# Optimization experiments

Hardware: AMD Instinct MI355X
Metric: run time of the kernel (lower is better)

The kernel has to match this reference:

```python
import jax, jax.numpy as jnp
import numpy as np

VOCAB, EMBED, HIDDEN = 32000, 256, 512
B, S = 64, 64


def setup_inputs() -> dict:
    key = jax.random.key(0)
    ks = jax.random.split(key, 10)
    target_seq = jax.random.randint(ks[0], (B, S), 0, VOCAB)
    context = jax.random.normal(ks[1], (B, HIDDEN), dtype=jnp.float32)
    h = jax.random.normal(ks[2], (B, HIDDEN), dtype=jnp.float32)
    c = jax.random.normal(ks[3], (B, HIDDEN), dtype=jnp.float32)
    # parameters (torch default-ish init scale)
    emb_table = jax.random.normal(ks[4], (VOCAB, EMBED), dtype=jnp.float32)
    k_lstm = 1.0 / np.sqrt(HIDDEN)
    w_ih = jax.random.uniform(ks[5], (4 * HIDDEN, EMBED + HIDDEN), minval=-k_lstm, maxval=k_lstm, dtype=jnp.float32)
    w_hh = jax.random.uniform(ks[6], (4 * HIDDEN, HIDDEN), minval=-k_lstm, maxval=k_lstm, dtype=jnp.float32)
    b_ih = jax.random.uniform(ks[7], (4 * HIDDEN,), minval=-k_lstm, maxval=k_lstm, dtype=jnp.float32)
    b_hh = jnp.zeros((4 * HIDDEN,), dtype=jnp.float32)
    k_fc = 1.0 / np.sqrt(2 * HIDDEN)
    w_fc = jax.random.uniform(ks[8], (VOCAB, 2 * HIDDEN), minval=-k_fc, maxval=k_fc, dtype=jnp.float32)
    b_fc = jax.random.uniform(ks[9], (VOCAB,), minval=-k_fc, maxval=k_fc, dtype=jnp.float32)
    return dict(target_seq=target_seq, context=context, h=h, c=c,
                emb_table=emb_table, w_ih=w_ih, w_hh=w_hh, b_ih=b_ih, b_hh=b_hh,
                w_fc=w_fc, b_fc=b_fc)


def _decode(target_seq, context, h, c, emb_table, w_ih, w_hh, b_ih, b_hh, w_fc, b_fc):
    # teacher_forcing_ratio = 1.0 -> input at step t is target_seq[:, t]
    emb = emb_table[target_seq]                                    # [B,S,E]
    ctx_t = jnp.broadcast_to(context[:, None, :], (emb.shape[0], emb.shape[1], context.shape[1]))
    lstm_in = jnp.concatenate([emb, ctx_t], axis=-1)               # [B,S,E+H]
    # precompute input-to-hidden part of gates for all steps
    pre = jnp.einsum('bsf,gf->bsg', lstm_in, w_ih) + b_ih + b_hh   # [B,S,4H]
    H = h.shape[1]

    def step(carry, pre_t):
        h_t, c_t = carry
        gates = pre_t + h_t @ w_hh.T                               # [B,4H]
        i, f, g, o = jnp.split(gates, 4, axis=-1)
        i, f, o = jax.nn.sigmoid(i), jax.nn.sigmoid(f), jax.nn.sigmoid(o)
        g = jnp.tanh(g)
        c_n = f * c_t + i * g
        h_n = o * jnp.tanh(c_n)
        return (h_n, c_n), h_n

    _, hs = jax.lax.scan(step, (h, c), jnp.swapaxes(pre, 0, 1))    # hs: [S,B,H]
    hs = jnp.swapaxes(hs, 0, 1)                                    # [B,S,H]
    out_in = jnp.concatenate([hs, ctx_t], axis=-1)                 # [B,S,2H]
    logits = jnp.einsum('bsf,vf->bsv', out_in, w_fc) + b_fc        # [B,S,V]
    return logits


def reference(target_seq, context, h, c, emb_table, w_ih, w_hh, b_ih, b_hh, w_fc, b_fc):
    return _decode(target_seq, context, h, c, emb_table, w_ih, w_hh, b_ih, b_hh, w_fc, b_fc)
```

## Files before the change

### kernel.cpp

```cpp
#include <hip/hip_runtime.h>
#include <hip/hip_bf16.h>

#define VOCAB 32000
#define EMBED 256
#define HIDDEN 512
#define BB 64
#define SS 64
#define M_ROWS (BB * SS)
#define G4 (4 * HIDDEN)
#define NBLK 16
#define NTOT 256
#define NTILE_N (VOCAB / 256)
#define CHUNK 5
#define NCHUNK (NTILE_N / CHUNK)
#define NITEM (SS * NCHUNK)

typedef __attribute__((ext_vector_type(8))) short short8v;
typedef __attribute__((ext_vector_type(4))) float float4v;
typedef __attribute__((ext_vector_type(4))) unsigned int uint4v;

__device__ __forceinline__ ushort f2bf(float f) {
    union { float f; unsigned u; } v; v.f = f;
    unsigned r = (v.u + 0x7FFFu + ((v.u >> 16) & 1u)) >> 16;
    return (ushort)r;
}

__device__ __forceinline__ float fast_tanh(float x) {
    float xc = fminf(fmaxf(x, -15.f), 15.f);
    float e = __expf(2.f * xc);
    return (e - 1.f) / (e + 1.f);
}

__device__ __forceinline__ void glds16(const ushort* g, ushort* l) {
    __builtin_amdgcn_global_load_lds(
        (const __attribute__((address_space(1))) unsigned int*)(const void*)g,
        (__attribute__((address_space(3))) unsigned int*)(void*)l, 16, 0, 0);
}

__global__ void k_conv_strided(const float* __restrict__ in, ushort* __restrict__ out,
                               int lg2cols, int instride, int n8) {
    int i = blockIdx.x * blockDim.x + threadIdx.x;
    int stride = gridDim.x * blockDim.x;
    int colmask = (1 << lg2cols) - 1;
    for (; i < n8; i += stride) {
        int i8 = i << 3;
        int row = i8 >> lg2cols, col = i8 & colmask;
        const float* src = in + (size_t)row * instride + col;
        float4 v0 = *(const float4*)src;
        float4 v1 = *(const float4*)(src + 4);
        short8v o;
        o[0] = (short)f2bf(v0.x); o[1] = (short)f2bf(v0.y);
        o[2] = (short)f2bf(v0.z); o[3] = (short)f2bf(v0.w);
        o[4] = (short)f2bf(v1.x); o[5] = (short)f2bf(v1.y);
        o[6] = (short)f2bf(v1.z); o[7] = (short)f2bf(v1.w);
        *(short8v*)(out + i8) = o;
    }
}

__global__ void k_build_emb(const int* __restrict__ tseq, const float* __restrict__ emb,
                            ushort* __restrict__ embbf) {
    int rid = blockIdx.x * 8 + (threadIdx.x >> 5);
    int c0 = (threadIdx.x & 31) * 8;
    int tok = tseq[rid];
    const float* src = emb + (size_t)tok * EMBED + c0;
    float4 v0 = *(const float4*)src;
    float4 v1 = *(const float4*)(src + 4);
    short8v o;
    o[0] = (short)f2bf(v0.x); o[1] = (short)f2bf(v0.y);
    o[2] = (short)f2bf(v0.z); o[3] = (short)f2bf(v0.w);
    o[4] = (short)f2bf(v1.x); o[5] = (short)f2bf(v1.y);
    o[6] = (short)f2bf(v1.z); o[7] = (short)f2bf(v1.w);
    *(short8v*)(embbf + (size_t)rid * EMBED + c0) = o;
}

__global__ void k_prep_small(const float* __restrict__ b_ih, const float* __restrict__ b_hh,
                             float* __restrict__ bias_pre,
                             const float* __restrict__ h0, ushort* __restrict__ hbufA,
                             const float* __restrict__ ctx, ushort* __restrict__ ctx_bf,
                             unsigned* __restrict__ ctrl) {
    int i = blockIdx.x * blockDim.x + threadIdx.x;
    if (i < 1024) ctrl[i] = 0;
    if (i < G4) bias_pre[i] = b_ih[i] + b_hh[i];
    if (i < BB * HIDDEN) {
        hbufA[i] = f2bf(h0[i]);
        ctx_bf[i] = f2bf(ctx[i]);
    }
}

__global__ __launch_bounds__(256) void k_gemm_smallM(
    const ushort* __restrict__ Abf, const float* __restrict__ Wf, int wstride,
    const float* __restrict__ bias, float* __restrict__ Cout, int N) {
    int t = threadIdx.x;
    int wv = t >> 6, lane = t & 63, lr = lane & 15, kg = lane >> 4;
    int bcol = blockIdx.x * 128;

    float4v acc[4][2];
#pragma unroll
    for (int m = 0; m < 4; m++)
#pragma unroll
        for (int n = 0; n < 2; n++) acc[m][n] = (float4v){0.f, 0.f, 0.f, 0.f};

#pragma unroll 4
    for (int ks = 0; ks < 16; ks++) {
        short8v a[4];
#pragma unroll
        for (int m = 0; m < 4; m++)
            a[m] = *(const short8v*)(Abf + (size_t)(m * 16 + lr) * 512 + ks * 32 + kg * 8);
        short8v w[2];
#pragma unroll
        for (int n = 0; n < 2; n++) {
            const float* src = Wf + (size_t)(bcol + wv * 32 + n * 16 + lr) * wstride + ks * 32 + kg * 8;
            float4 v0 = *(const float4*)src;
            float4 v1 = *(const float4*)(src + 4);
            short8v w8;
            w8[0] = (short)f2bf(v0.x); w8[1] = (short)f2bf(v0.y);
            w8[2] = (short)f2bf(v0.z); w8[3] = (short)f2bf(v0.w);
            w8[4] = (short)f2bf(v1.x); w8[5] = (short)f2bf(v1.y);
            w8[6] = (short)f2bf(v1.z); w8[7] = (short)f2bf(v1.w);
            w[n] = w8;
        }
#pragma unroll
        for (int m = 0; m < 4; m++)
#pragma unroll
            for (int n = 0; n < 2; n++)
                acc[m][n] = __builtin_amdgcn_mfma_f32_16x16x32_bf16(a[m], w[n], acc[m][n], 0, 0, 0);
    }

#pragma unroll
    for (int n = 0; n < 2; n++) {
        int col = bcol + wv * 32 + n * 16 + lr;
        float bv = bias[col];
#pragma unroll
        for (int m = 0; m < 4; m++) {
            int row = m * 16 + kg * 4;
#pragma unroll
            for (int j = 0; j < 4; j++)
                Cout[(size_t)(row + j) * N + col] = acc[m][n][j] + bv;
        }
    }
}

__global__ __launch_bounds__(512) void k_gemm_bf16(
    const ushort* __restrict__ A, const ushort* __restrict__ W,
    const float* __restrict__ rowbias, float* __restrict__ C,
    int M, int N, int K) {
    __shared__ ushort As[256 * 32];
    __shared__ ushort Ws[256 * 32];
    int t = threadIdx.x;

    int gx = N >> 8, gy = M >> 8;
    int nwg = gx * gy;
    int q = nwg >> 3, r = nwg & 7;
    int xcd = blockIdx.x & 7, idx = blockIdx.x >> 3;
    int wg = (xcd < r) ? xcd * (q + 1) + idx : r * (q + 1) + (xcd - r) * q + idx;
    const int SG = 4;
    int grp = wg / (gx * SG);
    int rem = wg % (gx * SG);
    int bx = rem / SG;
    int by = grp * SG + rem % SG;
    int brow = by * 256, bcol = bx * 256;

    int wave = t >> 6, lane = t & 63;
    int wr = wave >> 2, wc = wave & 3;
    int lr = lane & 15, kg = lane >> 4;

    float4v acc[8][4];
#pragma unroll
    for (int m = 0; m < 8; m++)
#pragma unroll
        for (int n = 0; n < 4; n++) acc[m][n] = (float4v){0.f, 0.f, 0.f, 0.f};

    int srow = t >> 2;
    int scol = (((t & 3) ^ (srow & 3))) * 8;
    const ushort* AgA = A + (size_t)(brow + srow) * K + scol;
    const ushort* AgB = A + (size_t)(brow + 128 + srow) * K + scol;
    const ushort* WgA = W + (size_t)(bcol + srow) * K + scol;
    const ushort* WgB = W + (size_t)(bcol + 128 + srow) * K + scol;
    ushort* ldsA0 = &As[(wave * 16) * 32];
    ushort* ldsA1 = &As[(128 + wave * 16) * 32];
    ushort* ldsW0 = &Ws[(wave * 16) * 32];
    ushort* ldsW1 = &Ws[(128 + wave * 16) * 32];

    for (int bk = 0; bk < K; bk += 32) {
        glds16(AgA + bk, ldsA0);
        glds16(AgB + bk, ldsA1);
        glds16(WgA + bk, ldsW0);
        glds16(WgB + bk, ldsW1);
        __syncthreads();
        short8v a[8], w[4];
#pragma unroll
        for (int m = 0; m < 8; m++) {
            int row = wr * 128 + m * 16 + lr;
            a[m] = *(const short8v*)&As[row * 32 + (kg ^ (row & 3)) * 8];
        }
#pragma unroll
        for (int n = 0; n < 4; n++) {
            int row = wc * 64 + n * 16 + lr;
            w[n] = *(const short8v*)&Ws[row * 32 + (kg ^ (row & 3)) * 8];
        }
#pragma unroll
        for (int m = 0; m < 8; m++)
#pragma unroll
            for (int n = 0; n < 4; n++)
                acc[m][n] = __builtin_amdgcn_mfma_f32_16x16x32_bf16(a[m], w[n], acc[m][n], 0, 0, 0);
        __syncthreads();
    }

#pragma unroll
    for (int n = 0; n < 4; n++) {
        int col = bcol + wc * 64 + n * 16 + lr;
#pragma unroll
        for (int m = 0; m < 8; m++) {
            int row = brow + wr * 128 + m * 16 + kg * 4;
            float bv = rowbias[(size_t)(row >> 6) * N + col];
            float4v v = acc[m][n];
#pragma unroll
            for (int j = 0; j < 4; j++)
                C[(size_t)(row + j) * N + col] = v[j] + bv;
        }
    }
}

__global__ __launch_bounds__(512) void k_mega(
    const float* __restrict__ pre, const float* __restrict__ w_hh,
    const float* __restrict__ c0,
    ushort* __restrict__ hbufA, ushort* __restrict__ hbufB,
    ushort* __restrict__ out_in, unsigned* __restrict__ ctrl,
    const ushort* __restrict__ Wfc, const float* __restrict__ ctxdot,
    float* __restrict__ Cout) {
    __shared__ __align__(16) char smem[99328];
    __shared__ int s_tile;
    unsigned* flags = ctrl;
    unsigned* queue = ctrl + 512;
    int t = threadIdx.x;
    int bid = blockIdx.x;
    int wave = t >> 6, lane = t & 63, lr = lane & 15, kg = lane >> 4;

    if (bid < NBLK) {
        ushort* h_lds = (ushort*)smem;
        float* G2 = (float*)(smem + 65536);
        char* hl = (char*)h_lds;
        int p = bid;
        int w = wave;
        int mh = w >> 2, cw2 = w & 3;

        short8v wfrag[2][16];
#pragma unroll
        for (int ci = 0; ci < 2; ci++) {
            const float* wrow = w_hh + (size_t)(cw2 * HIDDEN + p * 32 + ci * 16 + lr) * HIDDEN;
#pragma unroll
            for (int ks = 0; ks < 16; ks++) {
                const float* src = wrow + ks * 32 + kg * 8;
                short8v w8;
#pragma unroll
                for (int e = 0; e < 8; e++) w8[e] = (short)f2bf(src[e]);
                wfrag[ci][ks] = w8;
            }
        }

        int b = t >> 3, jj0 = (t & 7) * 4, jg0 = p * 32 + jj0;
        float4v c_reg = *(const float4v*)(c0 + (size_t)b * HIDDEN + jg0);
        float4v pv[4];
#pragma unroll
        for (int qg = 0; qg < 4; qg++)
            pv[qg] = *(const float4v*)(pre + (size_t)(b * SS) * G4 + qg * HIDDEN + jg0);

        for (int s = 0; s < SS; s++) {
            const ushort* hb = (s & 1) ? hbufB : hbufA;
            ushort* hn = (s & 1) ? hbufA : hbufB;

            if (s > 0) {
                const unsigned* fp = flags + (lane & 15) * 16;
                unsigned fv;
                do {
                    fv = __hip_atomic_load(fp, __ATOMIC_RELAXED, __HIP_MEMORY_SCOPE_AGENT);
                } while (__all((int)(fv >= (unsigned)s)) == 0);
            }

            {
                uint4v vb[8];
#pragma unroll
                for (int i = 0; i < 8; i++) {
                    int rr = w * 8 + i;
                    const void* src = hb + (size_t)rr * HIDDEN + lane * 8;
                    asm volatile("global_load_dwordx4 %0, %1, off sc0 sc1"
                                 : "=&v"(vb[i]) : "v"(src));
                }
                asm volatile("s_waitcnt vmcnt(0)" ::: "memory");
#pragma unroll
                for (int i = 0; i < 8; i++) {
                    int rr = w * 8 + i;
                    int off = (rr * 1024 + lane * 16) ^ ((rr & 7) << 4);
                    *(uint4v*)(hl + off) = vb[i];
                }
            }
            __syncthreads();

            float4v acc[2][2];
#pragma unroll
            for (int mi = 0; mi < 2; mi++)
#pragma unroll
                for (int ci = 0; ci < 2; ci++) acc[mi][ci] = (float4v){0.f, 0.f, 0.f, 0.f};
#pragma unroll
            for (int ks = 0; ks < 16; ks++) {
                short8v a[2];
#pragma unroll
                for (int mi = 0; mi < 2; mi++) {
                    int row = mh * 32 + mi * 16 + lr;
                    int off = (row * 1024 + ks * 64 + kg * 16) ^ ((row & 7) << 4);
                    a[mi] = *(const short8v*)(hl + off);
                }
#pragma unroll
                for (int mi = 0; mi < 2; mi++)
#pragma unroll
                    for (int ci = 0; ci < 2; ci++)
                        acc[mi][ci] = __builtin_amdgcn_mfma_f32_16x16x32_bf16(a[mi], wfrag[ci][ks], acc[mi][ci], 0, 0, 0);
            }
#pragma unroll
            for (int mi = 0; mi < 2; mi++)
#pragma unroll
                for (int ci = 0; ci < 2; ci++)
#pragma unroll
                    for (int rr = 0; rr < 4; rr++)
                        G2[(mh * 32 + mi * 16 + kg * 4 + rr) * 132 + cw2 * 32 + ci * 16 + lr] = acc[mi][ci][rr];
            __syncthreads();

            {
                float4v gq[4];
#pragma unroll
                for (int qg = 0; qg < 4; qg++) gq[qg] = *(const float4v*)&G2[b * 132 + qg * 32 + jj0];
                unsigned long long hv8 = 0;
#pragma unroll
                for (int e = 0; e < 4; e++) {
                    float xi = gq[0][e] + pv[0][e];
                    float xf = gq[1][e] + pv[1][e];
                    float xg = gq[2][e] + pv[2][e];
                    float xo = gq[3][e] + pv[3][e];
                    float ig = 1.f / (1.f + __expf(-xi));
                    float fg = 1.f / (1.f + __expf(-xf));
                    float gg = fast_tanh(xg);
                    float og = 1.f / (1.f + __expf(-xo));
                    float cn = fg * c_reg[e] + ig * gg;
                    float hv = og * fast_tanh(cn);
                    c_reg[e] = cn;
                    hv8 |= (unsigned long long)f2bf(hv) << (16 * e);
                }
                if (s + 1 < SS) {
                    __hip_atomic_store((unsigned long long*)(hn + (size_t)b * HIDDEN + jg0), hv8,
                                       __ATOMIC_RELAXED, __HIP_MEMORY_SCOPE_AGENT);
                }
                __hip_atomic_store((unsigned long long*)(out_in + (size_t)(s * BB + b) * HIDDEN + jg0), hv8,
                                   __ATOMIC_RELAXED, __HIP_MEMORY_SCOPE_AGENT);
                if (s + 1 < SS) {
#pragma unroll
                    for (int qg = 0; qg < 4; qg++)
                        pv[qg] = *(const float4v*)(pre + (size_t)(b * SS + s + 1) * G4 + qg * HIDDEN + jg0);
                }
            }

            __syncthreads();
            if (t == 0)
                __hip_atomic_store(flags + p * 16, (unsigned)(s + 1),
                                   __ATOMIC_RELEASE, __HIP_MEMORY_SCOPE_AGENT);
        }
    } else {
        ushort* As = (ushort*)smem;
        ushort* Ws = (ushort*)(smem + 65536);
        char* al = (char*)As;
        int srow = t >> 2;
        int scolW = ((t & 3) ^ (srow & 3)) * 8;
        ushort* ldsW0 = Ws + (wave * 16) * 32;
        ushort* ldsW1 = Ws + (128 + wave * 16) * 32;
        int last_rg = -1;

        for (;;) {
            __syncthreads();
            if (t == 0)
                s_tile = (int)__hip_atomic_fetch_add(queue, 1u, __ATOMIC_RELAXED, __HIP_MEMORY_SCOPE_AGENT);
            __syncthreads();
            int item = s_tile;
            if (item >= NITEM) break;
            int rg = item / NCHUNK;
            int ch = item % NCHUNK;

            if (rg != last_rg) {
                if (wave == 0) {
                    const unsigned* fp = flags + (lane & 15) * 16;
                    unsigned need = (unsigned)(rg + 1);
                    for (;;) {
                        unsigned fv = __hip_atomic_load(fp, __ATOMIC_RELAXED, __HIP_MEMORY_SCOPE_AGENT);
                        if (__all((int)(fv >= need))) break;
                        asm volatile("s_sleep 32");
                    }
                }
                __syncthreads();
                {
                    const ushort* Ab = out_in + (size_t)rg * 64 * HIDDEN;
                    uint4v vb[8];
#pragma unroll
                    for (int i = 0; i < 8; i++) {
                        int rr = wave * 8 + i;
                        const void* src = Ab + (size_t)rr * HIDDEN + lane * 8;
                        asm volatile("global_load_dwordx4 %0, %1, off sc0 sc1"
                                     : "=&v"(vb[i]) : "v"(src));
                    }
                    asm volatile("s_waitcnt vmcnt(0)" ::: "memory");
#pragma unroll
                    for (int i = 0; i < 8; i++) {
                        int rr = wave * 8 + i;
                        int off = (rr * 1024 + lane * 16) ^ ((rr & 7) << 4);
                        *(uint4v*)(al + off) = vb[i];
                    }
                }
                __syncthreads();
                last_rg = rg;
            }

            for (int q5 = 0; q5 < CHUNK; q5++) {
                int nt = ch * CHUNK + q5;
                int bcol = nt * 256;

                float4v acc[4][2];
#pragma unroll
                for (int m = 0; m < 4; m++)
#pragma unroll
                    for (int n = 0; n < 2; n++) acc[m][n] = (float4v){0.f, 0.f, 0.f, 0.f};

                const ushort* WgA = Wfc + (size_t)(bcol + srow) * HIDDEN + scolW;
                const ushort* WgB = WgA + (size_t)128 * HIDDEN;

                for (int ks = 0; ks < 16; ks++) {
                    glds16(WgA + ks * 32, ldsW0);
                    glds16(WgB + ks * 32, ldsW1);
                    __syncthreads();
                    short8v a[4], w[2];
#pragma unroll
                    for (int m = 0; m < 4; m++) {
                        int row = m * 16 + lr;
                        int off = (row * 1024 + ks * 64 + kg * 16) ^ ((row & 7) << 4);
                        a[m] = *(const short8v*)(al + off);
                    }
#pragma unroll
                    for (int n = 0; n < 2; n++) {
                        int wrow = wave * 32 + n * 16 + lr;
                        w[n] = *(const short8v*)&Ws[wrow * 32 + (kg ^ (wrow & 3)) * 8];
                    }
#pragma unroll
                    for (int m = 0; m < 4; m++)
#pragma unroll
                        for (int n = 0; n < 2; n++)
                            acc[m][n] = __builtin_amdgcn_mfma_f32_16x16x32_bf16(a[m], w[n], acc[m][n], 0, 0, 0);
                    __syncthreads();
                }

#pragma unroll
                for (int n = 0; n < 2; n++) {
                    int col = bcol + wave * 32 + n * 16 + lr;
#pragma unroll
                    for (int m = 0; m < 4; m++) {
                        int rbase = m * 16 + kg * 4;
#pragma unroll
                        for (int j = 0; j < 4; j++) {
                            int rl = rbase + j;
                            Cout[(size_t)(rl * 64 + rg) * VOCAB + col] =
                                acc[m][n][j] + ctxdot[(size_t)rl * VOCAB + col];
                        }
                    }
                }
            }
        }
    }
}

extern "C" void kernel_launch(void* const* d_in, const int* in_sizes, int n_in,
                              void* d_out, int out_size, void* d_ws, size_t ws_size,
                              hipStream_t stream) {
    const int*   tseq = (const int*)d_in[0];
    const float* ctx  = (const float*)d_in[1];
    const float* h0   = (const float*)d_in[2];
    const float* c0   = (const float*)d_in[3];
    const float* emb  = (const float*)d_in[4];
    const float* w_ih = (const float*)d_in[5];
    const float* w_hh = (const float*)d_in[6];
    const float* b_ih = (const float*)d_in[7];
    const float* b_hh = (const float*)d_in[8];
    const float* w_fc = (const float*)d_in[9];
    const float* b_fc = (const float*)d_in[10];
    float* out = (float*)d_out;

    char* wsb = (char*)d_ws;
    size_t off = 0;
    auto alloc = [&](size_t bytes) -> void* {
        void* ptr = wsb + off;
        off = (off + bytes + 255) & ~(size_t)255;
        return ptr;
    };
    ushort* emb_bf    = (ushort*)alloc((size_t)M_ROWS * EMBED * 2);
    ushort* w_ih_ebf  = (ushort*)alloc((size_t)G4 * EMBED * 2);
    ushort* w_fc_hbf  = (ushort*)alloc((size_t)VOCAB * HIDDEN * 2);
    ushort* out_in    = (ushort*)alloc((size_t)M_ROWS * HIDDEN * 2);
    float*  pre       = (float*)alloc((size_t)M_ROWS * G4 * 4);
    float*  prectx    = (float*)alloc((size_t)BB * G4 * 4);
    float*  ctxdot    = (float*)alloc((size_t)BB * VOCAB * 4);
    ushort* ctx_bf    = (ushort*)alloc((size_t)BB * HIDDEN * 2);
    ushort* hbufA     = (ushort*)alloc((size_t)BB * HIDDEN * 2);
    ushort* hbufB     = (ushort*)alloc((size_t)BB * HIDDEN * 2);
    float*  bias_pre  = (float*)alloc((size_t)G4 * 4);
    unsigned* ctrl    = (unsigned*)alloc(4096);

    k_conv_strided<<<256, 256, 0, stream>>>(w_ih, w_ih_ebf, 8, 768, G4 * EMBED / 8);
    k_conv_strided<<<2048, 256, 0, stream>>>(w_fc, w_fc_hbf, 9, 1024, VOCAB * HIDDEN / 8);
    k_build_emb<<<M_ROWS / 8, 256, 0, stream>>>(tseq, emb, emb_bf);
    k_prep_small<<<128, 256, 0, stream>>>(b_ih, b_hh, bias_pre, h0, hbufA, ctx, ctx_bf, ctrl);

    k_gemm_smallM<<<G4 / 128, 256, 0, stream>>>(ctx_bf, w_ih + 256, 768, bias_pre, prectx, G4);
    k_gemm_smallM<<<VOCAB / 128, 256, 0, stream>>>(ctx_bf, w_fc + 512, 1024, b_fc, ctxdot, VOCAB);

    k_gemm_bf16<<<dim3((G4 / 256) * (M_ROWS / 256)), 512, 0, stream>>>(
        emb_bf, w_ih_ebf, prectx, pre, M_ROWS, G4, EMBED);

    void* args[] = {(void*)&pre, (void*)&w_hh, (void*)&c0,
                    (void*)&hbufA, (void*)&hbufB, (void*)&out_in, (void*)&ctrl,
                    (void*)&w_fc_hbf, (void*)&ctxdot, (void*)&out};
    hipLaunchCooperativeKernel((void*)k_mega, dim3(NTOT), dim3(512), args, 0, stream);
}
```

Measured before the change: 715.5 us.

## Use 128-row output tiles over two timesteps with tapered work queue

```diff
diff --git a/kernel.cpp b/kernel.cpp
--- a/kernel.cpp
+++ b/kernel.cpp
@@ -11,9 +11,8 @@
 #define NBLK 16
 #define NTOT 256
 #define NTILE_N (VOCAB / 256)
-#define CHUNK 5
-#define NCHUNK (NTILE_N / CHUNK)
-#define NITEM (SS * NCHUNK)
+#define NHM 32
+#define NITEM 1000
 
 typedef __attribute__((ext_vector_type(8))) short short8v;
 typedef __attribute__((ext_vector_type(4))) float float4v;
@@ -228,7 +227,7 @@
     ushort* __restrict__ out_in, unsigned* __restrict__ ctrl,
     const ushort* __restrict__ Wfc, const float* __restrict__ ctxdot,
     float* __restrict__ Cout) {
-    __shared__ __align__(16) char smem[99328];
+    __shared__ __align__(16) char smem[147456];
     __shared__ int s_tile;
     unsigned* flags = ctrl;
     unsigned* queue = ctrl + 512;
@@ -365,13 +364,14 @@
         }
     } else {
         ushort* As = (ushort*)smem;
-        ushort* Ws = (ushort*)(smem + 65536);
+        ushort* Ws = (ushort*)(smem + 131072);
         char* al = (char*)As;
         int srow = t >> 2;
         int scolW = ((t & 3) ^ (srow & 3)) * 8;
         ushort* ldsW0 = Ws + (wave * 16) * 32;
         ushort* ldsW1 = Ws + (128 + wave * 16) * 32;
-        int last_rg = -1;
+        int wr = wave >> 2, wc = wave & 3;
+        int last_hm = -1, last_gated = -1;
 
         for (;;) {
             __syncthreads();
@@ -380,26 +380,32 @@
             __syncthreads();
             int item = s_tile;
             if (item >= NITEM) break;
-            int rg = item / NCHUNK;
-            int ch = item % NCHUNK;
-
-            if (rg != last_rg) {
+            int hm, nt0, cnt;
+            if (item < 750) { hm = item / 25; nt0 = (item % 25) * 5; cnt = 5; }
+            else { int j = item - 750; hm = 30 + j / 125; nt0 = j % 125; cnt = 1; }
+
+            int need = 2 * hm + 2;
+            if (need > last_gated) {
                 if (wave == 0) {
                     const unsigned* fp = flags + (lane & 15) * 16;
-                    unsigned need = (unsigned)(rg + 1);
                     for (;;) {
                         unsigned fv = __hip_atomic_load(fp, __ATOMIC_RELAXED, __HIP_MEMORY_SCOPE_AGENT);
-                        if (__all((int)(fv >= need))) break;
+                        if (__all((int)(fv >= (unsigned)need))) break;
                         asm volatile("s_sleep 32");
                     }
                 }
                 __syncthreads();
-                {
-                    const ushort* Ab = out_in + (size_t)rg * 64 * HIDDEN;
+                last_gated = need;
+            }
+
+            if (hm != last_hm) {
+                const ushort* Ab = out_in + (size_t)hm * 128 * HIDDEN;
+#pragma unroll
+                for (int half = 0; half < 2; half++) {
                     uint4v vb[8];
 #pragma unroll
                     for (int i = 0; i < 8; i++) {
-                        int rr = wave * 8 + i;
+                        int rr = wave * 16 + half * 8 + i;
                         const void* src = Ab + (size_t)rr * HIDDEN + lane * 8;
                         asm volatile("global_load_dwordx4 %0, %1, off sc0 sc1"
                                      : "=&v"(vb[i]) : "v"(src));
@@ -407,24 +413,24 @@
                     asm volatile("s_waitcnt vmcnt(0)" ::: "memory");
 #pragma unroll
                     for (int i = 0; i < 8; i++) {
-                        int rr = wave * 8 + i;
+                        int rr = wave * 16 + half * 8 + i;
                         int off = (rr * 1024 + lane * 16) ^ ((rr & 7) << 4);
                         *(uint4v*)(al + off) = vb[i];
                     }
                 }
                 __syncthreads();
-                last_rg = rg;
-            }
-
-            for (int q5 = 0; q5 < CHUNK; q5++) {
-                int nt = ch * CHUNK + q5;
+                last_hm = hm;
+            }
+
+            for (int q5 = 0; q5 < cnt; q5++) {
+                int nt = nt0 + q5;
                 int bcol = nt * 256;
 
-                float4v acc[4][2];
+                float4v acc[4][4];
 #pragma unroll
                 for (int m = 0; m < 4; m++)
 #pragma unroll
-                    for (int n = 0; n < 2; n++) acc[m][n] = (float4v){0.f, 0.f, 0.f, 0.f};
+                    for (int n = 0; n < 4; n++) acc[m][n] = (float4v){0.f, 0.f, 0.f, 0.f};
 
                 const ushort* WgA = Wfc + (size_t)(bcol + srow) * HIDDEN + scolW;
                 const ushort* WgB = WgA + (size_t)128 * HIDDEN;
@@ -433,37 +439,39 @@
                     glds16(WgA + ks * 32, ldsW0);
                     glds16(WgB + ks * 32, ldsW1);
                     __syncthreads();
-                    short8v a[4], w[2];
+                    short8v a[4], w[4];
 #pragma unroll
                     for (int m = 0; m < 4; m++) {
-                        int row = m * 16 + lr;
+                        int row = wr * 64 + m * 16 + lr;
                         int off = (row * 1024 + ks * 64 + kg * 16) ^ ((row & 7) << 4);
                         a[m] = *(const short8v*)(al + off);
                     }
 #pragma unroll
-                    for (int n = 0; n < 2; n++) {
-                        int wrow = wave * 32 + n * 16 + lr;
+                    for (int n = 0; n < 4; n++) {
+                        int wrow = wc * 64 + n * 16 + lr;
                         w[n] = *(const short8v*)&Ws[wrow * 32 + (kg ^ (wrow & 3)) * 8];
                     }
 #pragma unroll
                     for (int m = 0; m < 4; m++)
 #pragma unroll
-                        for (int n = 0; n < 2; n++)
+                        for (int n = 0; n < 4; n++)
                             acc[m][n] = __builtin_amdgcn_mfma_f32_16x16x32_bf16(a[m], w[n], acc[m][n], 0, 0, 0);
                     __syncthreads();
                 }
 
 #pragma unroll
-                for (int n = 0; n < 2; n++) {
-                    int col = bcol + wave * 32 + n * 16 + lr;
+                for (int n = 0; n < 4; n++) {
+                    int col = bcol + wc * 64 + n * 16 + lr;
 #pragma unroll
                     for (int m = 0; m < 4; m++) {
-                        int rbase = m * 16 + kg * 4;
+                        int rbase = wr * 64 + m * 16 + kg * 4;
 #pragma unroll
                         for (int j = 0; j < 4; j++) {
                             int rl = rbase + j;
-                            Cout[(size_t)(rl * 64 + rg) * VOCAB + col] =
-                                acc[m][n][j] + ctxdot[(size_t)rl * VOCAB + col];
+                            int bb = rl & 63;
+                            int ss = hm * 2 + (rl >> 6);
+                            float val = acc[m][n][j] + ctxdot[(size_t)bb * VOCAB + col];
+                            __builtin_nontemporal_store(val, &Cout[(size_t)(bb * 64 + ss) * VOCAB + col]);
                         }
                     }
                 }
```

Result: faster. 652.4 us (-8.8%).
